# Kernel tuning notes

Hardware: AMD Instinct MI355X
Metric: run time of the kernel (lower is better)

The kernel has to match this reference:

```python
import jax, jax.numpy as jnp
import numpy as np

B, C, H, W = 2, 320, 48, 48
HEADS, DIM_HEAD, NUM_FILTERS = 8, 64, 32
INNER = HEADS * DIM_HEAD  # 512
LN_EPS = 1e-05


def setup_inputs() -> dict:
    key = jax.random.key(0)
    ks = jax.random.split(key, 8)
    w = 0.02
    return {
        "hidden_states": jax.random.normal(ks[0], (B, C, H, W), jnp.float32),
        "encoder_hidden_states": jax.random.normal(ks[1], (B, C, H, W), jnp.float32),
        "Wq": jax.random.normal(ks[2], (C, INNER), jnp.float32) * w,
        "Wk": jax.random.normal(ks[3], (C, INNER), jnp.float32) * w,
        "Wv": jax.random.normal(ks[4], (C, INNER), jnp.float32) * w,
        "Wo": jax.random.normal(ks[5], (INNER, C), jnp.float32) * w,
        "bo": jnp.zeros((C,), jnp.float32),
        "ln_gamma": jnp.ones((C,), jnp.float32),
        "ln_beta": jnp.zeros((C,), jnp.float32),
        "ex_filters": jax.random.normal(ks[6], (NUM_FILTERS, INNER), jnp.float32),
        "dist_filters": jax.random.normal(ks[7], (NUM_FILTERS, INNER), jnp.float32),
        "scale": jnp.ones((1,), jnp.float32),  # learnable scale shadows dim_head**-0.5
    }


def _split_heads(t, heads):
    b, s, d = t.shape
    return t.reshape(b, s, heads, d // heads).transpose(0, 2, 1, 3)  # [b,h,s,dh]


def reference(hidden_states, encoder_hidden_states, Wq, Wk, Wv, Wo, bo,
              ln_gamma, ln_beta, ex_filters, dist_filters, scale):
    b, c, h, w = hidden_states.shape
    _, _, rh, rw = encoder_hidden_states.shape
    residual = hidden_states
    s = scale[0]

    hs = hidden_states.transpose(0, 2, 3, 1).reshape(b, h * w, c)        # [b, q, C]
    ehs = encoder_hidden_states.transpose(0, 2, 3, 1).reshape(b, rh * rw, c)

    # LayerNorm on encoder states
    mu = ehs.mean(-1, keepdims=True)
    var = jnp.mean((ehs - mu) ** 2, axis=-1, keepdims=True)
    ehs = (ehs - mu) * jax.lax.rsqrt(var + LN_EPS) * ln_gamma + ln_beta

    q = _split_heads(hs @ Wq, HEADS)    # [b,h,q,dh]
    k = _split_heads(ehs @ Wk, HEADS)   # [b,h,kv,dh]
    v = _split_heads(ehs @ Wv, HEADS)   # [b,h,kv,dh]
    ef = _split_heads(jnp.broadcast_to(ex_filters[None], (b,) + ex_filters.shape), HEADS)   # [b,h,F,dh]
    df = _split_heads(jnp.broadcast_to(dist_filters[None], (b,) + dist_filters.shape), HEADS)

    # spatial attention: softmax over kv positions
    spatial = jax.nn.softmax(jnp.einsum('bhfd,bhkd->bhfk', ef, k) * s, axis=-1)   # [b,h,F,kv]
    # channel attention: softmax over the filter axis (torch dim=1 of [B*h, F, q])
    channel = jax.nn.softmax(jnp.einsum('bhfd,bhqd->bhfq', df, q) * s, axis=2)    # [b,h,F,q]

    attn = jnp.einsum('bhfq,bhfk->bhqk', channel, spatial)                        # [b,h,q,kv]
    out = jnp.einsum('bhqk,bhkd->bhqd', attn, v)                                  # [b,h,q,dh]

    out = out.transpose(0, 2, 1, 3).reshape(b, h * w, INNER)
    out = out @ Wo + bo
    out = out.reshape(b, h, w, c).transpose(0, 3, 1, 2)
    return out + residual * s
```

## Files before the change

### kernel.cpp

```cpp
#include <hip/hip_runtime.h>
#include <math.h>

#define Bc 2
#define Cc 320
#define Pc 2304
#define HEADSc 8
#define DHc 64
#define INNERc 512
#define Fc 32
#define LN_EPS 1e-5f
#define CHUNKS 18
#define CHUNK_P 128

typedef __attribute__((ext_vector_type(8))) short bf16x8;
typedef __attribute__((ext_vector_type(4))) float f32x4;

static __device__ __forceinline__ ushort f2bf(float x) {
  uint u = __builtin_bit_cast(uint, x);
  u = (u + 0x7fffu + ((u >> 16) & 1u)) >> 16;
  return (ushort)u;
}

static __device__ void transpose_tile(const float* __restrict__ src,
                                      ushort* __restrict__ dst, int R, int C,
                                      int r0, int c0, int tid,
                                      float (*t)[65]) {
#pragma unroll
  for (int it = 0; it < 4; ++it) {
    int lin = it * 256 + tid;
    int rr = lin >> 4, c4 = lin & 15;
    float4 v = *(const float4*)(&src[(size_t)(r0 + rr) * C + c0 + c4 * 4]);
    t[rr][c4 * 4 + 0] = v.x; t[rr][c4 * 4 + 1] = v.y;
    t[rr][c4 * 4 + 2] = v.z; t[rr][c4 * 4 + 3] = v.w;
  }
  __syncthreads();
#pragma unroll
  for (int it = 0; it < 2; ++it) {
    int lin = it * 256 + tid;
    int cc = lin >> 3, r8 = lin & 7;
    ushort tmp[8];
#pragma unroll
    for (int j = 0; j < 8; ++j) tmp[j] = f2bf(t[r8 * 8 + j][cc]);
    *(uint4*)(&dst[(size_t)(c0 + cc) * R + r0 + r8 * 8]) = *(const uint4*)tmp;
  }
}

__global__ __launch_bounds__(256) void prep_all_kernel(
    const float* __restrict__ hs, const float* __restrict__ ehs,
    const float* __restrict__ gamma, const float* __restrict__ beta,
    const float* __restrict__ Wv, const float* __restrict__ Wo,
    const float* __restrict__ exf, const float* __restrict__ Wk,
    const float* __restrict__ dif, const float* __restrict__ Wq,
    ushort* __restrict__ hsT, ushort* __restrict__ ehsT,
    ushort* __restrict__ WvT, ushort* __restrict__ WoT,
    ushort* __restrict__ Gk, ushort* __restrict__ Gq) {
  __shared__ float smem[6448];
  int idx = blockIdx.x, tid = threadIdx.x;

  if (idx < 144) {
    int pt = idx % 36, z = idx / 36;
    int b = z & 1, which = z >> 1;
    int pos0 = pt * 64;
    const float* src = (which ? ehs : hs) + (size_t)b * Cc * Pc;
    ushort* dst = (which ? ehsT : hsT) + (size_t)b * Pc * Cc;
    float* t = smem;
    float* s1 = smem + 4160;
    float* s2 = smem + 4416;
    float* lmean = smem + 4672;
    float* lrstd = smem + 4736;
    int lane = tid & 63, g = tid >> 6;
    if (which) {
      const float* base = src + pos0 + lane;
      float sum = 0.f, sq = 0.f;
      for (int c = g * 80; c < g * 80 + 80; ++c) {
        float x = base[(size_t)c * Pc];
        sum += x; sq += x * x;
      }
      s1[g * 64 + lane] = sum; s2[g * 64 + lane] = sq;
      __syncthreads();
      if (tid < 64) {
        float ts = s1[tid] + s1[64 + tid] + s1[128 + tid] + s1[192 + tid];
        float tq = s2[tid] + s2[64 + tid] + s2[128 + tid] + s2[192 + tid];
        float mean = ts / (float)Cc;
        float var = tq / (float)Cc - mean * mean;
        lmean[tid] = mean;
        lrstd[tid] = rsqrtf(var + LN_EPS);
      }
      __syncthreads();
    }
    for (int ct = 0; ct < 5; ++ct) {
      int r0 = ct * 64;
#pragma unroll
      for (int it = 0; it < 4; ++it) {
        int lin = it * 256 + tid;
        int rr = lin >> 4, c4 = lin & 15;
        float4 v = *(const float4*)(&src[(size_t)(r0 + rr) * Pc + pos0 + c4 * 4]);
        t[rr * 65 + c4 * 4 + 0] = v.x; t[rr * 65 + c4 * 4 + 1] = v.y;
        t[rr * 65 + c4 * 4 + 2] = v.z; t[rr * 65 + c4 * 4 + 3] = v.w;
      }
      __syncthreads();
#pragma unroll
      for (int it = 0; it < 2; ++it) {
        int lin = it * 256 + tid;
        int cc = lin >> 3, r8 = lin & 7;
        float m_ = which ? lmean[cc] : 0.f, rs_ = which ? lrstd[cc] : 1.f;
        ushort tmp[8];
#pragma unroll
        for (int j = 0; j < 8; ++j) {
          int ch = r8 * 8 + j;
          float x = t[ch * 65 + cc];
          float val = which ? (x - m_) * rs_ * gamma[r0 + ch] + beta[r0 + ch] : x;
          tmp[j] = f2bf(val);
        }
        *(uint4*)(&dst[(size_t)(pos0 + cc) * Cc + r0 + r8 * 8]) =
            *(const uint4*)tmp;
      }
      __syncthreads();
    }
  } else {
    int idx2 = idx - 144;
    if (idx2 < 40) {
      transpose_tile(Wv, WvT, Cc, INNERc, (idx2 / 8) * 64, (idx2 % 8) * 64,
                     tid, (float(*)[65])smem);
    } else if (idx2 < 80) {
      int i = idx2 - 40;
      transpose_tile(Wo, WoT, INNERc, Cc, (i / 5) * 64, (i % 5) * 64, tid,
                     (float(*)[65])smem);
    } else {
      int i = idx2 - 80;
      int c0 = (i % 5) * 64, h = (i / 5) % 8, zz = i / 40;
      const float* filt = zz ? dif : exf;
      const float* W = zz ? Wq : Wk;
      ushort* G = zz ? Gq : Gk;
      float (*ef)[66] = (float(*)[66])smem;
      float (*wk)[65] = (float(*)[65])(smem + 32 * 66);
      for (int l = tid; l < Fc * DHc; l += 256) {
        int f = l >> 6, d = l & 63;
        ef[f][d] = filt[(size_t)f * INNERc + h * 64 + d];
      }
      for (int l = tid; l < 64 * DHc; l += 256) {
        int cc = l >> 6, d = l & 63;
        wk[cc][d] = W[(size_t)(c0 + cc) * INNERc + h * 64 + d];
      }
      __syncthreads();
      int f = tid >> 3, cbase = tid & 7;
      float acc[8] = {};
#pragma unroll
      for (int d4 = 0; d4 < DHc; d4 += 4) {
        float4 a = *(const float4*)(&ef[f][d4]);
#pragma unroll
        for (int j = 0; j < 8; ++j) {
          float4 b = *(const float4*)(&wk[cbase + j * 8][d4]);
          acc[j] += a.x * b.x + a.y * b.y + a.z * b.z + a.w * b.w;
        }
      }
#pragma unroll
      for (int j = 0; j < 8; ++j)
        G[(size_t)(h * Fc + f) * Cc + c0 + cbase + j * 8] = f2bf(acc[j]);
    }
  }
}

__global__ __launch_bounds__(256) void spatial_kernel(
    const ushort* __restrict__ Gk, const ushort* __restrict__ ehsT,
    const ushort* __restrict__ WvT, const float* __restrict__ scale_p,
    float* __restrict__ svp, float* __restrict__ mj, float* __restrict__ lj) {
  int c = blockIdx.x, h = blockIdx.y, b = blockIdx.z;
  int tid = threadIdx.x, lane = tid & 63, wv = tid >> 6;
  int l15 = lane & 15, kq = lane >> 4;
  int pos0 = c * CHUNK_P;
  int bh = b * HEADSc + h;
  float s = scale_p[0];

  __shared__ alignas(16) ushort As[96 * 64];
  __shared__ alignas(16) ushort Bs[128 * 64];
  __shared__ float Sq[32 * 132];
  __shared__ alignas(16) ushort P[32 * 136];
  __shared__ alignas(16) ushort Vs[64 * 136];

  const ushort* Av = WvT + (size_t)(h * 64) * Cc;
  const ushort* Ag = Gk + (size_t)(h * Fc) * Cc;
  const ushort* Bb = ehsT + ((size_t)b * Pc + pos0) * Cc;

  f32x4 acc[6][2] = {};
  for (int k0 = 0; k0 < Cc; k0 += 64) {
#pragma unroll
    for (int it = 0; it < 3; ++it) {
      int lin = it * 256 + tid;
      int row = lin >> 3, p = lin & 7;
      int lc = p ^ (row & 7);
      const ushort* sp = (row < 64) ? (Av + (size_t)row * Cc + k0 + lc * 8)
                                    : (Ag + (size_t)(row - 64) * Cc + k0 + lc * 8);
      *(uint4*)(&As[row * 64 + p * 8]) = *(const uint4*)sp;
    }
#pragma unroll
    for (int it = 0; it < 4; ++it) {
      int lin = it * 256 + tid;
      int row = lin >> 3, p = lin & 7;
      int lc = p ^ (row & 7);
      *(uint4*)(&Bs[row * 64 + p * 8]) =
          *(const uint4*)(Bb + (size_t)row * Cc + k0 + lc * 8);
    }
    __syncthreads();
#pragma unroll
    for (int ss = 0; ss < 2; ++ss) {
      bf16x8 af[6], bfr[2];
#pragma unroll
      for (int mt = 0; mt < 6; ++mt) {
        int m = mt * 16 + l15;
        int p = (ss * 4 + kq) ^ (m & 7);
        af[mt] = *(const bf16x8*)(&As[m * 64 + p * 8]);
      }
#pragma unroll
      for (int nt = 0; nt < 2; ++nt) {
        int n = wv * 32 + nt * 16 + l15;
        int p = (ss * 4 + kq) ^ (n & 7);
        bfr[nt] = *(const bf16x8*)(&Bs[n * 64 + p * 8]);
      }
#pragma unroll
      for (int mt = 0; mt < 6; ++mt)
#pragma unroll
        for (int nt = 0; nt < 2; ++nt)
          acc[mt][nt] = __builtin_amdgcn_mfma_f32_16x16x32_bf16(
              af[mt], bfr[nt], acc[mt][nt], 0, 0, 0);
    }
    __syncthreads();
  }
#pragma unroll
  for (int mt = 0; mt < 6; ++mt)
#pragma unroll
    for (int nt = 0; nt < 2; ++nt) {
      int col = wv * 32 + nt * 16 + l15;
#pragma unroll
      for (int r = 0; r < 4; ++r) {
        int row = mt * 16 + kq * 4 + r;
        if (mt < 4) Vs[row * 136 + col] = f2bf(acc[mt][nt][r]);
        else Sq[(row - 64) * 132 + col] = acc[mt][nt][r];
      }
    }
  __syncthreads();

  {
    int row = tid >> 3, sub = tid & 7;
    float vals[16];
    float m_ = -1e30f;
#pragma unroll
    for (int i = 0; i < 16; ++i) {
      vals[i] = s * Sq[row * 132 + sub * 16 + i];
      m_ = fmaxf(m_, vals[i]);
    }
    m_ = fmaxf(m_, __shfl_xor(m_, 1));
    m_ = fmaxf(m_, __shfl_xor(m_, 2));
    m_ = fmaxf(m_, __shfl_xor(m_, 4));
    float l_ = 0.f;
#pragma unroll
    for (int i = 0; i < 16; i += 2) {
      float e0 = __expf(vals[i] - m_);
      float e1 = __expf(vals[i + 1] - m_);
      l_ += e0 + e1;
      uint pk = (uint)f2bf(e0) | ((uint)f2bf(e1) << 16);
      *(uint*)(&P[row * 136 + sub * 16 + i]) = pk;
    }
    l_ += __shfl_xor(l_, 1);
    l_ += __shfl_xor(l_, 2);
    l_ += __shfl_xor(l_, 4);
    if (sub == 0) {
      mj[((size_t)c * 16 + bh) * Fc + row] = m_;
      lj[((size_t)c * 16 + bh) * Fc + row] = l_;
    }
  }
  __syncthreads();

  f32x4 acc2[2] = {};
#pragma unroll
  for (int ss = 0; ss < 4; ++ss) {
    bf16x8 af[2];
#pragma unroll
    for (int mt = 0; mt < 2; ++mt)
      af[mt] = *(const bf16x8*)(&P[(mt * 16 + l15) * 136 + ss * 32 + kq * 8]);
    bf16x8 bfr = *(const bf16x8*)(&Vs[(wv * 16 + l15) * 136 + ss * 32 + kq * 8]);
#pragma unroll
    for (int mt = 0; mt < 2; ++mt)
      acc2[mt] = __builtin_amdgcn_mfma_f32_16x16x32_bf16(af[mt], bfr, acc2[mt],
                                                         0, 0, 0);
  }
  float* op = svp + ((size_t)c * 16 + bh) * (Fc * DHc);
#pragma unroll
  for (int mt = 0; mt < 2; ++mt)
#pragma unroll
    for (int r = 0; r < 4; ++r)
      op[(mt * 16 + kq * 4 + r) * DHc + wv * 16 + l15] = acc2[mt][r];
}

__global__ __launch_bounds__(256) void sv_reduce_kernel(
    const float* __restrict__ svp, const float* __restrict__ mj,
    const float* __restrict__ lj, ushort* __restrict__ svT) {
  int idx = blockIdx.x * 256 + threadIdx.x;
  int d = idx & 63, fr = idx >> 6;
  int bh = fr >> 5, f = fr & 31;
  float m = -1e30f;
#pragma unroll
  for (int c = 0; c < CHUNKS; ++c)
    m = fmaxf(m, mj[((size_t)c * 16 + bh) * Fc + f]);
  float osum = 0.f, lsum = 0.f;
#pragma unroll
  for (int c = 0; c < CHUNKS; ++c) {
    float w = __expf(mj[((size_t)c * 16 + bh) * Fc + f] - m);
    osum += w * svp[((size_t)c * 16 + bh) * (Fc * DHc) + f * DHc + d];
    lsum += w * lj[((size_t)c * 16 + bh) * Fc + f];
  }
  svT[((size_t)bh * DHc + d) * Fc + f] = f2bf(osum / lsum);
}

__global__ __launch_bounds__(256) void channel_kernel(
    const ushort* __restrict__ Gq, const ushort* __restrict__ hsT,
    const ushort* __restrict__ svT, const float* __restrict__ scale_p,
    ushort* __restrict__ OAT) {
  int pb = blockIdx.x, hp = blockIdx.y, b = blockIdx.z;
  int pos0 = pb * 64;
  int tid = threadIdx.x, lane = tid & 63, wv = tid >> 6;
  int l15 = lane & 15, kq = lane >> 4;
  float s = scale_p[0];

  __shared__ alignas(16) ushort Aq[2][32 * 64];
  __shared__ alignas(16) ushort Bs[64 * 64];
  __shared__ float SO[64 * 68];
  __shared__ alignas(16) ushort Pt[64 * 40];
  __shared__ alignas(16) ushort svs[64 * 40];
  __shared__ float red[4 * 64];

  f32x4 acc[2][2] = {};
  const ushort* Bb = hsT + ((size_t)b * Pc + pos0) * Cc;
  for (int k0 = 0; k0 < Cc; k0 += 64) {
#pragma unroll
    for (int it = 0; it < 2; ++it) {
      int lin = it * 256 + tid;
      int hh = lin >> 8, row = (lin >> 3) & 31, p = lin & 7;
      int lc = p ^ (row & 7);
      *(uint4*)(&Aq[hh][row * 64 + p * 8]) = *(const uint4*)(
          Gq + (size_t)((hp * 2 + hh) * Fc + row) * Cc + k0 + lc * 8);
    }
#pragma unroll
    for (int it = 0; it < 2; ++it) {
      int lin = it * 256 + tid;
      int row = lin >> 3, p = lin & 7;
      int lc = p ^ (row & 7);
      *(uint4*)(&Bs[row * 64 + p * 8]) =
          *(const uint4*)(Bb + (size_t)row * Cc + k0 + lc * 8);
    }
    __syncthreads();
#pragma unroll
    for (int ss = 0; ss < 2; ++ss) {
      int n = wv * 16 + l15;
      int pb_ = (ss * 4 + kq) ^ (n & 7);
      bf16x8 bfr = *(const bf16x8*)(&Bs[n * 64 + pb_ * 8]);
#pragma unroll
      for (int hh = 0; hh < 2; ++hh)
#pragma unroll
        for (int mt = 0; mt < 2; ++mt) {
          int m = mt * 16 + l15;
          int pa = (ss * 4 + kq) ^ (m & 7);
          bf16x8 af = *(const bf16x8*)(&Aq[hh][m * 64 + pa * 8]);
          acc[hh][mt] = __builtin_amdgcn_mfma_f32_16x16x32_bf16(
              af, bfr, acc[hh][mt], 0, 0, 0);
        }
    }
    __syncthreads();
  }

  for (int hh = 0; hh < 2; ++hh) {
    int h = hp * 2 + hh;
#pragma unroll
    for (int mt = 0; mt < 2; ++mt)
#pragma unroll
      for (int r = 0; r < 4; ++r)
        SO[(mt * 16 + kq * 4 + r) * 68 + wv * 16 + l15] = acc[hh][mt][r];
    {
      int rr = tid >> 2, p = tid & 3;
      *(uint4*)(&svs[rr * 40 + p * 8]) = *(const uint4*)(
          svT + ((size_t)(b * HEADSc + h) * DHc + rr) * Fc + p * 8);
    }
    __syncthreads();
    {
      int pos = tid & 63, g = tid >> 6;
      float v8[8];
      float pm = -1e30f;
#pragma unroll
      for (int i = 0; i < 8; ++i) {
        v8[i] = s * SO[(g * 8 + i) * 68 + pos];
        pm = fmaxf(pm, v8[i]);
      }
      red[g * 64 + pos] = pm;
      __syncthreads();
      float m_ = fmaxf(fmaxf(red[pos], red[64 + pos]),
                       fmaxf(red[128 + pos], red[192 + pos]));
      __syncthreads();
      float ps = 0.f;
#pragma unroll
      for (int i = 0; i < 8; ++i) {
        v8[i] = __expf(v8[i] - m_);
        ps += v8[i];
      }
      red[g * 64 + pos] = ps;
      __syncthreads();
      float inv = 1.f / (red[pos] + red[64 + pos] + red[128 + pos] +
                         red[192 + pos]);
#pragma unroll
      for (int i = 0; i < 8; i += 2) {
        uint pk = (uint)f2bf(v8[i] * inv) | ((uint)f2bf(v8[i + 1] * inv) << 16);
        *(uint*)(&Pt[pos * 40 + g * 8 + i]) = pk;
      }
    }
    __syncthreads();
    {
      bf16x8 b_ = *(const bf16x8*)(&svs[(wv * 16 + l15) * 40 + kq * 8]);
      f32x4 acc3[4];
#pragma unroll
      for (int mt = 0; mt < 4; ++mt) {
        bf16x8 a_ = *(const bf16x8*)(&Pt[(mt * 16 + l15) * 40 + kq * 8]);
        f32x4 z = {0.f, 0.f, 0.f, 0.f};
        acc3[mt] = __builtin_amdgcn_mfma_f32_16x16x32_bf16(a_, b_, z, 0, 0, 0);
      }
#pragma unroll
      for (int mt = 0; mt < 4; ++mt)
#pragma unroll
        for (int r = 0; r < 4; ++r)
          SO[(mt * 16 + kq * 4 + r) * 68 + wv * 16 + l15] = acc3[mt][r];
    }
    __syncthreads();
#pragma unroll
    for (int it = 0; it < 2; ++it) {
      int lin = it * 256 + tid;
      int p = lin >> 3, c8 = lin & 7;
      ushort tmp[8];
#pragma unroll
      for (int j = 0; j < 8; ++j) tmp[j] = f2bf(SO[p * 68 + c8 * 8 + j]);
      *(uint4*)(&OAT[((size_t)b * Pc + pos0 + p) * INNERc + h * 64 + c8 * 8]) =
          *(const uint4*)tmp;
    }
    __syncthreads();
  }
}

__global__ __launch_bounds__(256) void gemm_mfma_kernel(
    const ushort* __restrict__ A, const ushort* __restrict__ Bt,
    float* __restrict__ Out, int K, int Mdim,
    const float* __restrict__ bias, const float* __restrict__ res,
    const float* __restrict__ scale_p) {
  int b = blockIdx.z;
  int n0 = blockIdx.x * 128, m0 = blockIdx.y * 64;
  int tid = threadIdx.x, lane = tid & 63, wv = tid >> 6;
  int l15 = lane & 15, kq = lane >> 4;
  __shared__ alignas(16) ushort As[64 * 64];
  __shared__ alignas(16) ushort Bs[128 * 64];
  const ushort* Ab = A + (size_t)m0 * K;
  const ushort* Bb = Bt + ((size_t)b * Pc + n0) * K;

  f32x4 acc[4][2] = {};
  for (int k0 = 0; k0 < K; k0 += 64) {
#pragma unroll
    for (int it = 0; it < 2; ++it) {
      int lin = it * 256 + tid;
      int row = lin >> 3, p = lin & 7;
      int lc = p ^ (row & 7);
      *(uint4*)(&As[row * 64 + p * 8]) =
          *(const uint4*)(Ab + (size_t)row * K + k0 + lc * 8);
    }
#pragma unroll
    for (int it = 0; it < 4; ++it) {
      int lin = it * 256 + tid;
      int row = lin >> 3, p = lin & 7;
      int lc = p ^ (row & 7);
      *(uint4*)(&Bs[row * 64 + p * 8]) =
          *(const uint4*)(Bb + (size_t)row * K + k0 + lc * 8);
    }
    __syncthreads();
#pragma unroll
    for (int ss = 0; ss < 2; ++ss) {
      bf16x8 af[4], bfr[2];
#pragma unroll
      for (int mt = 0; mt < 4; ++mt) {
        int m = mt * 16 + l15;
        int p = (ss * 4 + kq) ^ (m & 7);
        af[mt] = *(const bf16x8*)(&As[m * 64 + p * 8]);
      }
#pragma unroll
      for (int nt = 0; nt < 2; ++nt) {
        int n = wv * 32 + nt * 16 + l15;
        int p = (ss * 4 + kq) ^ (n & 7);
        bfr[nt] = *(const bf16x8*)(&Bs[n * 64 + p * 8]);
      }
#pragma unroll
      for (int mt = 0; mt < 4; ++mt)
#pragma unroll
        for (int nt = 0; nt < 2; ++nt)
          acc[mt][nt] = __builtin_amdgcn_mfma_f32_16x16x32_bf16(
              af[mt], bfr[nt], acc[mt][nt], 0, 0, 0);
    }
    __syncthreads();
  }
  float s = scale_p[0];
  float* Ob = Out + ((size_t)b * Mdim + m0) * Pc + n0;
  const float* rb = res + ((size_t)b * Mdim + m0) * Pc + n0;
#pragma unroll
  for (int mt = 0; mt < 4; ++mt)
#pragma unroll
    for (int nt = 0; nt < 2; ++nt) {
      int ncol = wv * 32 + nt * 16 + l15;
#pragma unroll
      for (int r = 0; r < 4; ++r) {
        int m = mt * 16 + kq * 4 + r;
        Ob[(size_t)m * Pc + ncol] =
            acc[mt][nt][r] + bias[m0 + m] + s * rb[(size_t)m * Pc + ncol];
      }
    }
}

extern "C" void kernel_launch(void* const* d_in, const int* in_sizes, int n_in,
                              void* d_out, int out_size, void* d_ws, size_t ws_size,
                              hipStream_t stream) {
  const float* hs    = (const float*)d_in[0];
  const float* ehs   = (const float*)d_in[1];
  const float* Wq    = (const float*)d_in[2];
  const float* Wk    = (const float*)d_in[3];
  const float* Wv    = (const float*)d_in[4];
  const float* Wo    = (const float*)d_in[5];
  const float* bo    = (const float*)d_in[6];
  const float* gamma = (const float*)d_in[7];
  const float* beta  = (const float*)d_in[8];
  const float* exf   = (const float*)d_in[9];
  const float* dif   = (const float*)d_in[10];
  const float* scale = (const float*)d_in[11];
  float* out = (float*)d_out;

  float* ws = (float*)d_ws;
  float* svp = ws;
  float* mj  = svp + 589824;
  float* lj  = mj + 9216;
  ushort* hsT  = (ushort*)(lj + 9216);
  ushort* ehsT = hsT + 1474560;
  ushort* WvT  = ehsT + 1474560;
  ushort* WoT  = WvT + 163840;
  ushort* Gk   = WoT + 163840;
  ushort* Gq   = Gk + 81920;
  ushort* svT  = Gq + 81920;
  ushort* OAT  = svT + 32768;

  prep_all_kernel<<<dim3(304), dim3(256), 0, stream>>>(
      hs, ehs, gamma, beta, Wv, Wo, exf, Wk, dif, Wq,
      hsT, ehsT, WvT, WoT, Gk, Gq);
  spatial_kernel<<<dim3(CHUNKS, HEADSc, Bc), dim3(256), 0, stream>>>(
      Gk, ehsT, WvT, scale, svp, mj, lj);
  sv_reduce_kernel<<<dim3(128), dim3(256), 0, stream>>>(svp, mj, lj, svT);
  channel_kernel<<<dim3(Pc / 64, HEADSc / 2, Bc), dim3(256), 0, stream>>>(
      Gq, hsT, svT, scale, OAT);
  gemm_mfma_kernel<<<dim3(Pc / 128, Cc / 64, Bc), dim3(256), 0, stream>>>(
      WoT, OAT, out, INNERc, Cc, bo, hs, scale);
}
```

Measured before the change: 138.4 us.

## Fuse sv_reduce into spatial via last-block atomics; merge channel and output GEMM

```diff
diff --git a/kernel.cpp b/kernel.cpp
--- a/kernel.cpp
+++ b/kernel.cpp
@@ -53,10 +53,15 @@
     const float* __restrict__ dif, const float* __restrict__ Wq,
     ushort* __restrict__ hsT, ushort* __restrict__ ehsT,
     ushort* __restrict__ WvT, ushort* __restrict__ WoT,
-    ushort* __restrict__ Gk, ushort* __restrict__ Gq) {
+    ushort* __restrict__ Gk, ushort* __restrict__ Gq,
+    int* __restrict__ counters) {
   __shared__ float smem[6448];
   int idx = blockIdx.x, tid = threadIdx.x;
 
+  if (idx == 304) {
+    if (tid < 64) counters[tid] = 0;
+    return;
+  }
   if (idx < 144) {
     int pt = idx % 36, z = idx / 36;
     int b = z & 1, which = z >> 1;
@@ -164,7 +169,8 @@
 __global__ __launch_bounds__(256) void spatial_kernel(
     const ushort* __restrict__ Gk, const ushort* __restrict__ ehsT,
     const ushort* __restrict__ WvT, const float* __restrict__ scale_p,
-    float* __restrict__ svp, float* __restrict__ mj, float* __restrict__ lj) {
+    float* __restrict__ svp, float* __restrict__ mj, float* __restrict__ lj,
+    ushort* __restrict__ svT, int* __restrict__ cnt_sp) {
   int c = blockIdx.x, h = blockIdx.y, b = blockIdx.z;
   int tid = threadIdx.x, lane = tid & 63, wv = tid >> 6;
   int l15 = lane & 15, kq = lane >> 4;
@@ -177,6 +183,7 @@
   __shared__ float Sq[32 * 132];
   __shared__ alignas(16) ushort P[32 * 136];
   __shared__ alignas(16) ushort Vs[64 * 136];
+  __shared__ int lastflag;
 
   const ushort* Av = WvT + (size_t)(h * 64) * Cc;
   const ushort* Ag = Gk + (size_t)(h * Fc) * Cc;
@@ -290,230 +297,251 @@
 #pragma unroll
     for (int r = 0; r < 4; ++r)
       op[(mt * 16 + kq * 4 + r) * DHc + wv * 16 + l15] = acc2[mt][r];
+
+  __threadfence();
+  if (tid == 0) {
+    int old = __hip_atomic_fetch_add(&cnt_sp[bh], 1, __ATOMIC_ACQ_REL,
+                                     __HIP_MEMORY_SCOPE_AGENT);
+    lastflag = (old == CHUNKS - 1);
+  }
+  __syncthreads();
+  if (!lastflag) return;
+  __threadfence();
+  for (int l = tid; l < Fc * DHc; l += 256) {
+    int d = l & 63, f = l >> 6;
+    float m = -1e30f;
+#pragma unroll
+    for (int cc = 0; cc < CHUNKS; ++cc)
+      m = fmaxf(m, mj[((size_t)cc * 16 + bh) * Fc + f]);
+    float osum = 0.f, lsum = 0.f;
+#pragma unroll
+    for (int cc = 0; cc < CHUNKS; ++cc) {
+      float w = __expf(mj[((size_t)cc * 16 + bh) * Fc + f] - m);
+      osum += w * svp[((size_t)cc * 16 + bh) * (Fc * DHc) + f * DHc + d];
+      lsum += w * lj[((size_t)cc * 16 + bh) * Fc + f];
+    }
+    svT[((size_t)bh * DHc + d) * Fc + f] = f2bf(osum / lsum);
+  }
 }
 
-__global__ __launch_bounds__(256) void sv_reduce_kernel(
-    const float* __restrict__ svp, const float* __restrict__ mj,
-    const float* __restrict__ lj, ushort* __restrict__ svT) {
-  int idx = blockIdx.x * 256 + threadIdx.x;
-  int d = idx & 63, fr = idx >> 6;
-  int bh = fr >> 5, f = fr & 31;
-  float m = -1e30f;
-#pragma unroll
-  for (int c = 0; c < CHUNKS; ++c)
-    m = fmaxf(m, mj[((size_t)c * 16 + bh) * Fc + f]);
-  float osum = 0.f, lsum = 0.f;
-#pragma unroll
-  for (int c = 0; c < CHUNKS; ++c) {
-    float w = __expf(mj[((size_t)c * 16 + bh) * Fc + f] - m);
-    osum += w * svp[((size_t)c * 16 + bh) * (Fc * DHc) + f * DHc + d];
-    lsum += w * lj[((size_t)c * 16 + bh) * Fc + f];
-  }
-  svT[((size_t)bh * DHc + d) * Fc + f] = f2bf(osum / lsum);
-}
-
-__global__ __launch_bounds__(256) void channel_kernel(
+__global__ __launch_bounds__(256) void chanfinal_kernel(
     const ushort* __restrict__ Gq, const ushort* __restrict__ hsT,
     const ushort* __restrict__ svT, const float* __restrict__ scale_p,
-    ushort* __restrict__ OAT) {
-  int pb = blockIdx.x, hp = blockIdx.y, b = blockIdx.z;
-  int pos0 = pb * 64;
-  int tid = threadIdx.x, lane = tid & 63, wv = tid >> 6;
+    ushort* __restrict__ OAT, const ushort* __restrict__ WoT,
+    const float* __restrict__ bo, const float* __restrict__ res,
+    float* __restrict__ Out, int* __restrict__ cnt_cf) {
+  __shared__ char smem[45056] __attribute__((aligned(16)));
+  int idx = blockIdx.x, tid = threadIdx.x;
+  int lane = tid & 63, wv = tid >> 6;
   int l15 = lane & 15, kq = lane >> 4;
   float s = scale_p[0];
 
-  __shared__ alignas(16) ushort Aq[2][32 * 64];
-  __shared__ alignas(16) ushort Bs[64 * 64];
-  __shared__ float SO[64 * 68];
-  __shared__ alignas(16) ushort Pt[64 * 40];
-  __shared__ alignas(16) ushort svs[64 * 40];
-  __shared__ float red[4 * 64];
-
-  f32x4 acc[2][2] = {};
-  const ushort* Bb = hsT + ((size_t)b * Pc + pos0) * Cc;
-  for (int k0 = 0; k0 < Cc; k0 += 64) {
-#pragma unroll
-    for (int it = 0; it < 2; ++it) {
-      int lin = it * 256 + tid;
-      int hh = lin >> 8, row = (lin >> 3) & 31, p = lin & 7;
-      int lc = p ^ (row & 7);
-      *(uint4*)(&Aq[hh][row * 64 + p * 8]) = *(const uint4*)(
-          Gq + (size_t)((hp * 2 + hh) * Fc + row) * Cc + k0 + lc * 8);
-    }
-#pragma unroll
-    for (int it = 0; it < 2; ++it) {
-      int lin = it * 256 + tid;
-      int row = lin >> 3, p = lin & 7;
-      int lc = p ^ (row & 7);
-      *(uint4*)(&Bs[row * 64 + p * 8]) =
-          *(const uint4*)(Bb + (size_t)row * Cc + k0 + lc * 8);
+  if (idx < 288) {
+    int pb = idx % 36, hp = (idx / 36) % 4, b = idx / 144;
+    int pos0 = pb * 64;
+    ushort (*Aq)[32 * 64] = (ushort(*)[32 * 64])smem;
+    ushort* Bs = (ushort*)(smem + 8192);
+    float* SO = (float*)(smem + 16384);
+    ushort* Pt = (ushort*)(smem + 33792);
+    ushort* svs = (ushort*)(smem + 38912);
+    float* red = (float*)(smem + 44032);
+
+    f32x4 acc[2][2] = {};
+    const ushort* Bb = hsT + ((size_t)b * Pc + pos0) * Cc;
+    for (int k0 = 0; k0 < Cc; k0 += 64) {
+#pragma unroll
+      for (int it = 0; it < 2; ++it) {
+        int lin = it * 256 + tid;
+        int hh = lin >> 8, row = (lin >> 3) & 31, p = lin & 7;
+        int lc = p ^ (row & 7);
+        *(uint4*)(&Aq[hh][row * 64 + p * 8]) = *(const uint4*)(
+            Gq + (size_t)((hp * 2 + hh) * Fc + row) * Cc + k0 + lc * 8);
+      }
+#pragma unroll
+      for (int it = 0; it < 2; ++it) {
+        int lin = it * 256 + tid;
+        int row = lin >> 3, p = lin & 7;
+        int lc = p ^ (row & 7);
+        *(uint4*)(&Bs[row * 64 + p * 8]) =
+            *(const uint4*)(Bb + (size_t)row * Cc + k0 + lc * 8);
+      }
+      __syncthreads();
+#pragma unroll
+      for (int ss = 0; ss < 2; ++ss) {
+        int n = wv * 16 + l15;
+        int pb_ = (ss * 4 + kq) ^ (n & 7);
+        bf16x8 bfr = *(const bf16x8*)(&Bs[n * 64 + pb_ * 8]);
+#pragma unroll
+        for (int hh = 0; hh < 2; ++hh)
+#pragma unroll
+          for (int mt = 0; mt < 2; ++mt) {
+            int m = mt * 16 + l15;
+            int pa = (ss * 4 + kq) ^ (m & 7);
+            bf16x8 af = *(const bf16x8*)(&Aq[hh][m * 64 + pa * 8]);
+            acc[hh][mt] = __builtin_amdgcn_mfma_f32_16x16x32_bf16(
+                af, bfr, acc[hh][mt], 0, 0, 0);
+          }
+      }
+      __syncthreads();
+    }
+
+    for (int hh = 0; hh < 2; ++hh) {
+      int h = hp * 2 + hh;
+#pragma unroll
+      for (int mt = 0; mt < 2; ++mt)
+#pragma unroll
+        for (int r = 0; r < 4; ++r)
+          SO[(mt * 16 + kq * 4 + r) * 68 + wv * 16 + l15] = acc[hh][mt][r];
+      {
+        int rr = tid >> 2, p = tid & 3;
+        *(uint4*)(&svs[rr * 40 + p * 8]) = *(const uint4*)(
+            svT + ((size_t)(b * HEADSc + h) * DHc + rr) * Fc + p * 8);
+      }
+      __syncthreads();
+      {
+        int pos = tid & 63, g = tid >> 6;
+        float v8[8];
+        float pm = -1e30f;
+#pragma unroll
+        for (int i = 0; i < 8; ++i) {
+          v8[i] = s * SO[(g * 8 + i) * 68 + pos];
+          pm = fmaxf(pm, v8[i]);
+        }
+        red[g * 64 + pos] = pm;
+        __syncthreads();
+        float m_ = fmaxf(fmaxf(red[pos], red[64 + pos]),
+                         fmaxf(red[128 + pos], red[192 + pos]));
+        __syncthreads();
+        float ps = 0.f;
+#pragma unroll
+        for (int i = 0; i < 8; ++i) {
+          v8[i] = __expf(v8[i] - m_);
+          ps += v8[i];
+        }
+        red[g * 64 + pos] = ps;
+        __syncthreads();
+        float inv = 1.f / (red[pos] + red[64 + pos] + red[128 + pos] +
+                           red[192 + pos]);
+#pragma unroll
+        for (int i = 0; i < 8; i += 2) {
+          uint pk = (uint)f2bf(v8[i] * inv) |
+                    ((uint)f2bf(v8[i + 1] * inv) << 16);
+          *(uint*)(&Pt[pos * 40 + g * 8 + i]) = pk;
+        }
+      }
+      __syncthreads();
+      {
+        bf16x8 b_ = *(const bf16x8*)(&svs[(wv * 16 + l15) * 40 + kq * 8]);
+        f32x4 acc3[4];
+#pragma unroll
+        for (int mt = 0; mt < 4; ++mt) {
+          bf16x8 a_ = *(const bf16x8*)(&Pt[(mt * 16 + l15) * 40 + kq * 8]);
+          f32x4 z = {0.f, 0.f, 0.f, 0.f};
+          acc3[mt] =
+              __builtin_amdgcn_mfma_f32_16x16x32_bf16(a_, b_, z, 0, 0, 0);
+        }
+#pragma unroll
+        for (int mt = 0; mt < 4; ++mt)
+#pragma unroll
+          for (int r = 0; r < 4; ++r)
+            SO[(mt * 16 + kq * 4 + r) * 68 + wv * 16 + l15] = acc3[mt][r];
+      }
+      __syncthreads();
+#pragma unroll
+      for (int it = 0; it < 2; ++it) {
+        int lin = it * 256 + tid;
+        int p = lin >> 3, c8 = lin & 7;
+        ushort tmp[8];
+#pragma unroll
+        for (int j = 0; j < 8; ++j) tmp[j] = f2bf(SO[p * 68 + c8 * 8 + j]);
+        *(uint4*)(&OAT[((size_t)b * Pc + pos0 + p) * INNERc + h * 64 +
+                       c8 * 8]) = *(const uint4*)tmp;
+      }
+      __syncthreads();
+    }
+    __threadfence();
+    if (tid == 0)
+      __hip_atomic_fetch_add(&cnt_cf[b * 18 + (pb >> 1)], 1, __ATOMIC_RELEASE,
+                             __HIP_MEMORY_SCOPE_AGENT);
+  } else {
+    int i = idx - 288;
+    int x = i % 18, y = (i / 18) % 5, b = i / 90;
+    int n0 = x * 128, m0 = y * 64;
+    const int K = INNERc;
+    ushort* As = (ushort*)smem;
+    ushort* Bs = (ushort*)(smem + 8192);
+
+    if (tid == 0) {
+      int iters = 0;
+      while (__hip_atomic_load(&cnt_cf[b * 18 + x], __ATOMIC_ACQUIRE,
+                               __HIP_MEMORY_SCOPE_AGENT) < 8 &&
+             iters < 100000000) {
+        __builtin_amdgcn_s_sleep(8);
+        ++iters;
+      }
     }
     __syncthreads();
-#pragma unroll
-    for (int ss = 0; ss < 2; ++ss) {
-      int n = wv * 16 + l15;
-      int pb_ = (ss * 4 + kq) ^ (n & 7);
-      bf16x8 bfr = *(const bf16x8*)(&Bs[n * 64 + pb_ * 8]);
-#pragma unroll
-      for (int hh = 0; hh < 2; ++hh)
-#pragma unroll
-        for (int mt = 0; mt < 2; ++mt) {
+
+    const ushort* Ab = WoT + (size_t)m0 * K;
+    const ushort* Bb = OAT + ((size_t)b * Pc + n0) * K;
+    f32x4 acc[4][2] = {};
+    for (int k0 = 0; k0 < K; k0 += 64) {
+#pragma unroll
+      for (int it = 0; it < 2; ++it) {
+        int lin = it * 256 + tid;
+        int row = lin >> 3, p = lin & 7;
+        int lc = p ^ (row & 7);
+        *(uint4*)(&As[row * 64 + p * 8]) =
+            *(const uint4*)(Ab + (size_t)row * K + k0 + lc * 8);
+      }
+#pragma unroll
+      for (int it = 0; it < 4; ++it) {
+        int lin = it * 256 + tid;
+        int row = lin >> 3, p = lin & 7;
+        int lc = p ^ (row & 7);
+        *(uint4*)(&Bs[row * 64 + p * 8]) =
+            *(const uint4*)(Bb + (size_t)row * K + k0 + lc * 8);
+      }
+      __syncthreads();
+#pragma unroll
+      for (int ss = 0; ss < 2; ++ss) {
+        bf16x8 af[4], bfr[2];
+#pragma unroll
+        for (int mt = 0; mt < 4; ++mt) {
           int m = mt * 16 + l15;
-          int pa = (ss * 4 + kq) ^ (m & 7);
-          bf16x8 af = *(const bf16x8*)(&Aq[hh][m * 64 + pa * 8]);
-          acc[hh][mt] = __builtin_amdgcn_mfma_f32_16x16x32_bf16(
-              af, bfr, acc[hh][mt], 0, 0, 0);
-        }
-    }
-    __syncthreads();
-  }
-
-  for (int hh = 0; hh < 2; ++hh) {
-    int h = hp * 2 + hh;
-#pragma unroll
-    for (int mt = 0; mt < 2; ++mt)
-#pragma unroll
-      for (int r = 0; r < 4; ++r)
-        SO[(mt * 16 + kq * 4 + r) * 68 + wv * 16 + l15] = acc[hh][mt][r];
-    {
-      int rr = tid >> 2, p = tid & 3;
-      *(uint4*)(&svs[rr * 40 + p * 8]) = *(const uint4*)(
-          svT + ((size_t)(b * HEADSc + h) * DHc + rr) * Fc + p * 8);
-    }
-    __syncthreads();
-    {
-      int pos = tid & 63, g = tid >> 6;
-      float v8[8];
-      float pm = -1e30f;
-#pragma unroll
-      for (int i = 0; i < 8; ++i) {
-        v8[i] = s * SO[(g * 8 + i) * 68 + pos];
-        pm = fmaxf(pm, v8[i]);
-      }
-      red[g * 64 + pos] = pm;
-      __syncthreads();
-      float m_ = fmaxf(fmaxf(red[pos], red[64 + pos]),
-                       fmaxf(red[128 + pos], red[192 + pos]));
-      __syncthreads();
-      float ps = 0.f;
-#pragma unroll
-      for (int i = 0; i < 8; ++i) {
-        v8[i] = __expf(v8[i] - m_);
-        ps += v8[i];
-      }
-      red[g * 64 + pos] = ps;
-      __syncthreads();
-      float inv = 1.f / (red[pos] + red[64 + pos] + red[128 + pos] +
-                         red[192 + pos]);
-#pragma unroll
-      for (int i = 0; i < 8; i += 2) {
-        uint pk = (uint)f2bf(v8[i] * inv) | ((uint)f2bf(v8[i + 1] * inv) << 16);
-        *(uint*)(&Pt[pos * 40 + g * 8 + i]) = pk;
-      }
-    }
-    __syncthreads();
-    {
-      bf16x8 b_ = *(const bf16x8*)(&svs[(wv * 16 + l15) * 40 + kq * 8]);
-      f32x4 acc3[4];
-#pragma unroll
-      for (int mt = 0; mt < 4; ++mt) {
-        bf16x8 a_ = *(const bf16x8*)(&Pt[(mt * 16 + l15) * 40 + kq * 8]);
-        f32x4 z = {0.f, 0.f, 0.f, 0.f};
-        acc3[mt] = __builtin_amdgcn_mfma_f32_16x16x32_bf16(a_, b_, z, 0, 0, 0);
-      }
-#pragma unroll
-      for (int mt = 0; mt < 4; ++mt)
-#pragma unroll
-        for (int r = 0; r < 4; ++r)
-          SO[(mt * 16 + kq * 4 + r) * 68 + wv * 16 + l15] = acc3[mt][r];
-    }
-    __syncthreads();
-#pragma unroll
-    for (int it = 0; it < 2; ++it) {
-      int lin = it * 256 + tid;
-      int p = lin >> 3, c8 = lin & 7;
-      ushort tmp[8];
-#pragma unroll
-      for (int j = 0; j < 8; ++j) tmp[j] = f2bf(SO[p * 68 + c8 * 8 + j]);
-      *(uint4*)(&OAT[((size_t)b * Pc + pos0 + p) * INNERc + h * 64 + c8 * 8]) =
-          *(const uint4*)tmp;
-    }
-    __syncthreads();
-  }
-}
-
-__global__ __launch_bounds__(256) void gemm_mfma_kernel(
-    const ushort* __restrict__ A, const ushort* __restrict__ Bt,
-    float* __restrict__ Out, int K, int Mdim,
-    const float* __restrict__ bias, const float* __restrict__ res,
-    const float* __restrict__ scale_p) {
-  int b = blockIdx.z;
-  int n0 = blockIdx.x * 128, m0 = blockIdx.y * 64;
-  int tid = threadIdx.x, lane = tid & 63, wv = tid >> 6;
-  int l15 = lane & 15, kq = lane >> 4;
-  __shared__ alignas(16) ushort As[64 * 64];
-  __shared__ alignas(16) ushort Bs[128 * 64];
-  const ushort* Ab = A + (size_t)m0 * K;
-  const ushort* Bb = Bt + ((size_t)b * Pc + n0) * K;
-
-  f32x4 acc[4][2] = {};
-  for (int k0 = 0; k0 < K; k0 += 64) {
-#pragma unroll
-    for (int it = 0; it < 2; ++it) {
-      int lin = it * 256 + tid;
-      int row = lin >> 3, p = lin & 7;
-      int lc = p ^ (row & 7);
-      *(uint4*)(&As[row * 64 + p * 8]) =
-          *(const uint4*)(Ab + (size_t)row * K + k0 + lc * 8);
-    }
-#pragma unroll
-    for (int it = 0; it < 4; ++it) {
-      int lin = it * 256 + tid;
-      int row = lin >> 3, p = lin & 7;
-      int lc = p ^ (row & 7);
-      *(uint4*)(&Bs[row * 64 + p * 8]) =
-          *(const uint4*)(Bb + (size_t)row * K + k0 + lc * 8);
-    }
-    __syncthreads();
-#pragma unroll
-    for (int ss = 0; ss < 2; ++ss) {
-      bf16x8 af[4], bfr[2];
-#pragma unroll
-      for (int mt = 0; mt < 4; ++mt) {
-        int m = mt * 16 + l15;
-        int p = (ss * 4 + kq) ^ (m & 7);
-        af[mt] = *(const bf16x8*)(&As[m * 64 + p * 8]);
-      }
+          int p = (ss * 4 + kq) ^ (m & 7);
+          af[mt] = *(const bf16x8*)(&As[m * 64 + p * 8]);
+        }
+#pragma unroll
+        for (int nt = 0; nt < 2; ++nt) {
+          int n = wv * 32 + nt * 16 + l15;
+          int p = (ss * 4 + kq) ^ (n & 7);
+          bfr[nt] = *(const bf16x8*)(&Bs[n * 64 + p * 8]);
+        }
+#pragma unroll
+        for (int mt = 0; mt < 4; ++mt)
+#pragma unroll
+          for (int nt = 0; nt < 2; ++nt)
+            acc[mt][nt] = __builtin_amdgcn_mfma_f32_16x16x32_bf16(
+                af[mt], bfr[nt], acc[mt][nt], 0, 0, 0);
+      }
+      __syncthreads();
+    }
+    float* Ob = Out + ((size_t)b * Cc + m0) * Pc + n0;
+    const float* rb = res + ((size_t)b * Cc + m0) * Pc + n0;
+#pragma unroll
+    for (int mt = 0; mt < 4; ++mt)
 #pragma unroll
       for (int nt = 0; nt < 2; ++nt) {
-        int n = wv * 32 + nt * 16 + l15;
-        int p = (ss * 4 + kq) ^ (n & 7);
-        bfr[nt] = *(const bf16x8*)(&Bs[n * 64 + p * 8]);
-      }
-#pragma unroll
-      for (int mt = 0; mt < 4; ++mt)
-#pragma unroll
-        for (int nt = 0; nt < 2; ++nt)
-          acc[mt][nt] = __builtin_amdgcn_mfma_f32_16x16x32_bf16(
-              af[mt], bfr[nt], acc[mt][nt], 0, 0, 0);
-    }
-    __syncthreads();
-  }
-  float s = scale_p[0];
-  float* Ob = Out + ((size_t)b * Mdim + m0) * Pc + n0;
-  const float* rb = res + ((size_t)b * Mdim + m0) * Pc + n0;
-#pragma unroll
-  for (int mt = 0; mt < 4; ++mt)
-#pragma unroll
-    for (int nt = 0; nt < 2; ++nt) {
-      int ncol = wv * 32 + nt * 16 + l15;
-#pragma unroll
-      for (int r = 0; r < 4; ++r) {
-        int m = mt * 16 + kq * 4 + r;
-        Ob[(size_t)m * Pc + ncol] =
-            acc[mt][nt][r] + bias[m0 + m] + s * rb[(size_t)m * Pc + ncol];
-      }
-    }
+        int ncol = wv * 32 + nt * 16 + l15;
+#pragma unroll
+        for (int r = 0; r < 4; ++r) {
+          int m = mt * 16 + kq * 4 + r;
+          Ob[(size_t)m * Pc + ncol] =
+              acc[mt][nt][r] + bo[m0 + m] + s * rb[(size_t)m * Pc + ncol];
+        }
+      }
+  }
 }
 
 extern "C" void kernel_launch(void* const* d_in, const int* in_sizes, int n_in,
@@ -537,7 +565,8 @@
   float* svp = ws;
   float* mj  = svp + 589824;
   float* lj  = mj + 9216;
-  ushort* hsT  = (ushort*)(lj + 9216);
+  int* counters = (int*)(lj + 9216);
+  ushort* hsT  = (ushort*)(counters + 64);
   ushort* ehsT = hsT + 1474560;
   ushort* WvT  = ehsT + 1474560;
   ushort* WoT  = WvT + 163840;
@@ -545,15 +574,14 @@
   ushort* Gq   = Gk + 81920;
   ushort* svT  = Gq + 81920;
   ushort* OAT  = svT + 32768;
-
-  prep_all_kernel<<<dim3(304), dim3(256), 0, stream>>>(
+  int* cnt_sp = counters;
+  int* cnt_cf = counters + 16;
+
+  prep_all_kernel<<<dim3(305), dim3(256), 0, stream>>>(
       hs, ehs, gamma, beta, Wv, Wo, exf, Wk, dif, Wq,
-      hsT, ehsT, WvT, WoT, Gk, Gq);
+      hsT, ehsT, WvT, WoT, Gk, Gq, counters);
   spatial_kernel<<<dim3(CHUNKS, HEADSc, Bc), dim3(256), 0, stream>>>(
-      Gk, ehsT, WvT, scale, svp, mj, lj);
-  sv_reduce_kernel<<<dim3(128), dim3(256), 0, stream>>>(svp, mj, lj, svT);
-  channel_kernel<<<dim3(Pc / 64, HEADSc / 2, Bc), dim3(256), 0, stream>>>(
-      Gq, hsT, svT, scale, OAT);
-  gemm_mfma_kernel<<<dim3(Pc / 128, Cc / 64, Bc), dim3(256), 0, stream>>>(
-      WoT, OAT, out, INNERc, Cc, bo, hs, scale);
+      Gk, ehsT, WvT, scale, svp, mj, lj, svT, cnt_sp);
+  chanfinal_kernel<<<dim3(288 + 180), dim3(256), 0, stream>>>(
+      Gq, hsT, svT, scale, OAT, WoT, bo, hs, out, cnt_cf);
 }
```

Result: slower. 221.1 us (+59.8%).

## Fuse split-softmax reduction into spatial kernel via last-block atomic counter

Applied to the files above, without the earlier changes.

```diff
diff --git a/kernel.cpp b/kernel.cpp
--- a/kernel.cpp
+++ b/kernel.cpp
@@ -53,10 +53,15 @@
     const float* __restrict__ dif, const float* __restrict__ Wq,
     ushort* __restrict__ hsT, ushort* __restrict__ ehsT,
     ushort* __restrict__ WvT, ushort* __restrict__ WoT,
-    ushort* __restrict__ Gk, ushort* __restrict__ Gq) {
+    ushort* __restrict__ Gk, ushort* __restrict__ Gq,
+    int* __restrict__ counters) {
   __shared__ float smem[6448];
   int idx = blockIdx.x, tid = threadIdx.x;
 
+  if (idx == 304) {
+    if (tid < 64) counters[tid] = 0;
+    return;
+  }
   if (idx < 144) {
     int pt = idx % 36, z = idx / 36;
     int b = z & 1, which = z >> 1;
@@ -164,7 +169,8 @@
 __global__ __launch_bounds__(256) void spatial_kernel(
     const ushort* __restrict__ Gk, const ushort* __restrict__ ehsT,
     const ushort* __restrict__ WvT, const float* __restrict__ scale_p,
-    float* __restrict__ svp, float* __restrict__ mj, float* __restrict__ lj) {
+    float* __restrict__ svp, float* __restrict__ mj, float* __restrict__ lj,
+    ushort* __restrict__ svT, int* __restrict__ cnt_sp) {
   int c = blockIdx.x, h = blockIdx.y, b = blockIdx.z;
   int tid = threadIdx.x, lane = tid & 63, wv = tid >> 6;
   int l15 = lane & 15, kq = lane >> 4;
@@ -177,6 +183,7 @@
   __shared__ float Sq[32 * 132];
   __shared__ alignas(16) ushort P[32 * 136];
   __shared__ alignas(16) ushort Vs[64 * 136];
+  __shared__ int lastflag;
 
   const ushort* Av = WvT + (size_t)(h * 64) * Cc;
   const ushort* Ag = Gk + (size_t)(h * Fc) * Cc;
@@ -290,26 +297,31 @@
 #pragma unroll
     for (int r = 0; r < 4; ++r)
       op[(mt * 16 + kq * 4 + r) * DHc + wv * 16 + l15] = acc2[mt][r];
-}
-
-__global__ __launch_bounds__(256) void sv_reduce_kernel(
-    const float* __restrict__ svp, const float* __restrict__ mj,
-    const float* __restrict__ lj, ushort* __restrict__ svT) {
-  int idx = blockIdx.x * 256 + threadIdx.x;
-  int d = idx & 63, fr = idx >> 6;
-  int bh = fr >> 5, f = fr & 31;
-  float m = -1e30f;
-#pragma unroll
-  for (int c = 0; c < CHUNKS; ++c)
-    m = fmaxf(m, mj[((size_t)c * 16 + bh) * Fc + f]);
-  float osum = 0.f, lsum = 0.f;
-#pragma unroll
-  for (int c = 0; c < CHUNKS; ++c) {
-    float w = __expf(mj[((size_t)c * 16 + bh) * Fc + f] - m);
-    osum += w * svp[((size_t)c * 16 + bh) * (Fc * DHc) + f * DHc + d];
-    lsum += w * lj[((size_t)c * 16 + bh) * Fc + f];
-  }
-  svT[((size_t)bh * DHc + d) * Fc + f] = f2bf(osum / lsum);
+
+  __threadfence();
+  if (tid == 0) {
+    int old = __hip_atomic_fetch_add(&cnt_sp[bh], 1, __ATOMIC_ACQ_REL,
+                                     __HIP_MEMORY_SCOPE_AGENT);
+    lastflag = (old == CHUNKS - 1);
+  }
+  __syncthreads();
+  if (!lastflag) return;
+  __threadfence();
+  for (int l = tid; l < Fc * DHc; l += 256) {
+    int d = l & 63, f = l >> 6;
+    float m = -1e30f;
+#pragma unroll
+    for (int cc = 0; cc < CHUNKS; ++cc)
+      m = fmaxf(m, mj[((size_t)cc * 16 + bh) * Fc + f]);
+    float osum = 0.f, lsum = 0.f;
+#pragma unroll
+    for (int cc = 0; cc < CHUNKS; ++cc) {
+      float w = __expf(mj[((size_t)cc * 16 + bh) * Fc + f] - m);
+      osum += w * svp[((size_t)cc * 16 + bh) * (Fc * DHc) + f * DHc + d];
+      lsum += w * lj[((size_t)cc * 16 + bh) * Fc + f];
+    }
+    svT[((size_t)bh * DHc + d) * Fc + f] = f2bf(osum / lsum);
+  }
 }
 
 __global__ __launch_bounds__(256) void channel_kernel(
@@ -537,7 +549,8 @@
   float* svp = ws;
   float* mj  = svp + 589824;
   float* lj  = mj + 9216;
-  ushort* hsT  = (ushort*)(lj + 9216);
+  int* counters = (int*)(lj + 9216);
+  ushort* hsT  = (ushort*)(counters + 64);
   ushort* ehsT = hsT + 1474560;
   ushort* WvT  = ehsT + 1474560;
   ushort* WoT  = WvT + 163840;
@@ -545,13 +558,13 @@
   ushort* Gq   = Gk + 81920;
   ushort* svT  = Gq + 81920;
   ushort* OAT  = svT + 32768;
-
-  prep_all_kernel<<<dim3(304), dim3(256), 0, stream>>>(
+  int* cnt_sp = counters;
+
+  prep_all_kernel<<<dim3(305), dim3(256), 0, stream>>>(
       hs, ehs, gamma, beta, Wv, Wo, exf, Wk, dif, Wq,
-      hsT, ehsT, WvT, WoT, Gk, Gq);
+      hsT, ehsT, WvT, WoT, Gk, Gq, counters);
   spatial_kernel<<<dim3(CHUNKS, HEADSc, Bc), dim3(256), 0, stream>>>(
-      Gk, ehsT, WvT, scale, svp, mj, lj);
-  sv_reduce_kernel<<<dim3(128), dim3(256), 0, stream>>>(svp, mj, lj, svT);
+      Gk, ehsT, WvT, scale, svp, mj, lj, svT, cnt_sp);
   channel_kernel<<<dim3(Pc / 64, HEADSc / 2, Bc), dim3(256), 0, stream>>>(
       Gq, hsT, svT, scale, OAT);
   gemm_mfma_kernel<<<dim3(Pc / 128, Cc / 64, Bc), dim3(256), 0, stream>>>(
```

New measurement: 176.2 us. 1.27x slower.
